# Performance work log

Measured on AMD Instinct MI355X. Metric: run time of the kernel, lower is better.

The kernel has to match this reference:

```python
import jax, jax.numpy as jnp
import numpy as np

B, P, V, E, F = 4, 8, 2048, 2048, 4096
BIG = 1e10  # stand-in for +inf that keeps gradients clean


def setup_inputs() -> dict:
    key = jax.random.key(0)
    ks = jax.random.split(key, 8)
    xs = jax.random.normal(ks[0], (B, V, 3), jnp.float32)
    # Projection matrices: random rows for x/y, third (depth) row kept near
    # [0,0,0,2] so the perspective divide is well conditioned for randn verts.
    pm = 0.5 * jax.random.normal(ks[1], (P, 3, 4), jnp.float32)
    pm = pm.at[:, 2, :3].set(0.01 * jax.random.normal(ks[2], (P, 3), jnp.float32))
    pm = pm.at[:, 2, 3].set(2.0)
    edgemaps = jax.random.normal(ks[3], (B, P, E, 2), jnp.float32)
    edgemap_lengths = jax.random.randint(ks[4], (B, P), E // 2, E + 1)
    boundary_mask = jax.random.randint(ks[5], (B, P, V), 0, 2).astype(bool)
    faces = jax.random.randint(ks[6], (B, F, 3), 0, V)
    target_volumes = 10.0 * jax.random.normal(ks[7], (B,), jnp.float32)
    return dict(xs=xs, projmatrices=pm, edgemaps=edgemaps,
                edgemap_lengths=edgemap_lengths, boundary_mask=boundary_mask,
                faces=faces, target_volumes=target_volumes)


def _silhouette_chamfer(xs, projmatrices, edgemaps, edgemap_lengths, boundary_mask):
    b, v, _ = xs.shape
    xh = jnp.concatenate([xs, jnp.ones((b, v, 1), xs.dtype)], axis=-1)  # [B,V,4]
    proj = jnp.einsum('pij,bvj->bpvi', projmatrices, xh)               # [B,P,V,3]
    pts = proj[..., :2] / proj[..., 2:3]                               # [B,P,V,2]
    e = edgemaps.shape[2]
    d2 = (jnp.sum(pts * pts, -1)[..., :, None]
          + jnp.sum(edgemaps * edgemaps, -1)[..., None, :]
          - 2.0 * jnp.einsum('bpvc,bpec->bpve', pts, edgemaps))
    yvalid = jnp.arange(e)[None, None, :] < edgemap_lengths[..., None]  # [B,P,E]
    d2 = jnp.where(yvalid[:, :, None, :], d2, jnp.asarray(BIG, d2.dtype))
    mins = jnp.min(d2, axis=-1)                                        # [B,P,V]
    xm = boundary_mask.astype(d2.dtype)
    # point_reduction='mean' over valid boundary points per projection,
    # batch_reduction='mean' over the P projections of each mesh.
    per_proj = jnp.sum(mins * xm, -1) / jnp.maximum(jnp.sum(xm, -1), 1.0)  # [B,P]
    return jnp.mean(per_proj, axis=-1)                                 # [B]


def _volume_constraint(xs, faces, target_volumes):
    b = xs.shape[0]
    fv = xs[jnp.arange(b)[:, None, None], faces]   # [B,F,3,3] gather face verts
    v0, v1, v2 = fv[:, :, 0], fv[:, :, 1], fv[:, :, 2]
    face_vols = jnp.sum(jnp.cross(v0, v1) * v2, axis=-1) / 6.0  # [B,F]
    vols = jnp.abs(jnp.sum(face_vols, axis=-1))                 # scatter-add per mesh
    return (vols - target_volumes) ** 2                          # [B]


def reference(xs, projmatrices, edgemaps, edgemap_lengths, boundary_mask, faces, target_volumes):
    chamfer = _silhouette_chamfer(xs, projmatrices, edgemaps, edgemap_lengths, boundary_mask)
    vol_error = _volume_constraint(xs, faces, target_volumes)
    return chamfer, vol_error
```

## Files before the change

### kernel.cpp

```cpp
#include <hip/hip_runtime.h>

#define NB 4
#define NP 8
#define NV 2048
#define NE 2048
#define NF 4096
#define BIGV 1.0e10f
#define NCHUNK 16
#define ECHUNK 128
#define NCOMBO (NB * NP)

#define MINPART_FLOATS (NCOMBO * NCHUNK * NV)

__global__ __launch_bounds__(256) void fused_k1(
    const float* __restrict__ xs, const float* __restrict__ pm,
    const float* __restrict__ edgemaps, const int* __restrict__ elen,
    const int* __restrict__ faces, float* __restrict__ minpart,
    float* __restrict__ volpart)
{
    __shared__ float4 eds[ECHUNK];
    __shared__ float red[4];
    const int tid = threadIdx.x;
    const int bid = blockIdx.x;

    if (bid < 512) {
        const int combo  = bid >> 4;
        const int echunk = bid & 15;
        const int b = combo >> 3;
        const int p = combo & 7;

        if (tid < ECHUNK) {
            const int e   = echunk * ECHUNK + tid;
            const int len = elen[combo];
            float ex = edgemaps[((size_t)combo * NE + e) * 2 + 0];
            float ey = edgemaps[((size_t)combo * NE + e) * 2 + 1];
            float e2;
            if (e < len) {
                e2 = ex * ex + ey * ey;
            } else {
                ex = 0.0f; ey = 0.0f; e2 = BIGV;
            }
            eds[tid] = make_float4(ex, ey, e2, 0.0f);
        }

        const float* M = pm + p * 12;
        const float m00 = M[0], m01 = M[1], m02 = M[2],  m03 = M[3];
        const float m10 = M[4], m11 = M[5], m12 = M[6],  m13 = M[7];
        const float m20 = M[8], m21 = M[9], m22 = M[10], m23 = M[11];

        float px2[8], py2[8], v2[8], mn[8];
        #pragma unroll
        for (int i = 0; i < 8; i++) {
            const int v = tid + (i << 8);
            const float x = xs[((size_t)b * NV + v) * 3 + 0];
            const float y = xs[((size_t)b * NV + v) * 3 + 1];
            const float z = xs[((size_t)b * NV + v) * 3 + 2];
            const float r0 = m00 * x + m01 * y + m02 * z + m03;
            const float r1 = m10 * x + m11 * y + m12 * z + m13;
            const float r2 = m20 * x + m21 * y + m22 * z + m23;
            const float inv = 1.0f / r2;
            const float px = r0 * inv;
            const float py = r1 * inv;
            px2[i] = -2.0f * px;
            py2[i] = -2.0f * py;
            v2[i]  = px * px + py * py;
            mn[i]  = 3.0e38f;
        }
        __syncthreads();

        #pragma unroll 4
        for (int k = 0; k < ECHUNK; k++) {
            const float4 ed = eds[k];
            #pragma unroll
            for (int i = 0; i < 8; i++)
                mn[i] = fminf(mn[i], fmaf(py2[i], ed.y, fmaf(px2[i], ed.x, ed.z)));
        }

        float* dst = minpart + ((size_t)(combo * NCHUNK + echunk)) * NV;
        #pragma unroll
        for (int i = 0; i < 8; i++)
            dst[tid + (i << 8)] = mn[i] + v2[i];
    } else {
        const int j = bid - 512;
        const int b = j >> 4;
        const int f = ((j & 15) << 8) + tid;
        const int* fc = faces + ((size_t)b * NF + f) * 3;
        const int i0 = fc[0], i1 = fc[1], i2 = fc[2];
        const float* xb = xs + (size_t)b * NV * 3;
        const float ax = xb[i0 * 3 + 0], ay = xb[i0 * 3 + 1], az = xb[i0 * 3 + 2];
        const float bx = xb[i1 * 3 + 0], by = xb[i1 * 3 + 1], bz = xb[i1 * 3 + 2];
        const float cx = xb[i2 * 3 + 0], cy = xb[i2 * 3 + 1], cz = xb[i2 * 3 + 2];
        const float crx = ay * bz - az * by;
        const float cry = az * bx - ax * bz;
        const float crz = ax * by - ay * bx;
        float fv = (crx * cx + cry * cy + crz * cz) * (1.0f / 6.0f);

        #pragma unroll
        for (int off = 32; off > 0; off >>= 1) fv += __shfl_down(fv, off);
        const int lane = tid & 63, w = tid >> 6;
        if (lane == 0) red[w] = fv;
        __syncthreads();
        if (tid == 0) volpart[j] = red[0] + red[1] + red[2] + red[3];
    }
}

__global__ __launch_bounds__(256) void fused_k2(
    const float* __restrict__ minpart, const void* __restrict__ maskp,
    float* __restrict__ percombo)
{
    __shared__ float reds[4], redc[4];
    const int tid = threadIdx.x;
    const int lane = tid & 63, w = tid >> 6;
    const int combo = blockIdx.x;

    const int* mi = (const int*)maskp;
    const unsigned char* mb = (const unsigned char*)maskp;
    bool as_int = true;
    #pragma unroll
    for (int k = 0; k < 16; k++)
        if (((const unsigned*)maskp)[k] > 1u) as_int = false;

    const float* base = minpart + (size_t)combo * NCHUNK * NV;
    float s = 0.0f, c = 0.0f;
    #pragma unroll
    for (int i = 0; i < 8; i++) {
        const int v = tid + (i << 8);
        float m = base[v];
        #pragma unroll
        for (int ch = 1; ch < NCHUNK; ch++)
            m = fminf(m, base[ch * NV + v]);
        const size_t mix = (size_t)combo * NV + v;
        const float msk = as_int ? (mi[mix] ? 1.0f : 0.0f)
                                 : (mb[mix] ? 1.0f : 0.0f);
        s += m * msk;
        c += msk;
    }
    #pragma unroll
    for (int off = 32; off > 0; off >>= 1) {
        s += __shfl_down(s, off);
        c += __shfl_down(c, off);
    }
    if (lane == 0) { reds[w] = s; redc[w] = c; }
    __syncthreads();
    if (tid == 0) {
        const float S = reds[0] + reds[1] + reds[2] + reds[3];
        const float C = redc[0] + redc[1] + redc[2] + redc[3];
        percombo[combo] = S / fmaxf(C, 1.0f);
    }
}

__global__ __launch_bounds__(64) void fused_k3(
    const float* __restrict__ percombo, const float* __restrict__ volpart,
    const float* __restrict__ tv, float* __restrict__ out)
{
    const int b = threadIdx.x;
    if (b < NB) {
        float a = 0.0f;
        #pragma unroll
        for (int p = 0; p < NP; p++) a += percombo[b * NP + p];
        out[b] = a * (1.0f / NP);
        float vs = 0.0f;
        #pragma unroll
        for (int k = 0; k < 16; k++) vs += volpart[b * 16 + k];
        const float d = fabsf(vs) - tv[b];
        out[4 + b] = d * d;
    }
}

extern "C" void kernel_launch(void* const* d_in, const int* in_sizes, int n_in,
                              void* d_out, int out_size, void* d_ws, size_t ws_size,
                              hipStream_t stream)
{
    const float* xs       = (const float*)d_in[0];
    const float* pm       = (const float*)d_in[1];
    const float* edgemaps = (const float*)d_in[2];
    const int*   elen     = (const int*)d_in[3];
    const void*  mask     = d_in[4];
    const int*   faces    = (const int*)d_in[5];
    const float* tv       = (const float*)d_in[6];
    float* out = (float*)d_out;

    float* minpart  = (float*)d_ws;
    float* volpart  = minpart + MINPART_FLOATS;
    float* percombo = volpart + 64;

    fused_k1<<<dim3(576), dim3(256), 0, stream>>>(xs, pm, edgemaps, elen, faces, minpart, volpart);
    fused_k2<<<dim3(NCOMBO), dim3(256), 0, stream>>>(minpart, mask, percombo);
    fused_k3<<<dim3(1), dim3(64), 0, stream>>>(percombo, volpart, tv, out);
}
```

Baseline: 85.93 us.

## Split work by vertex chunk and reduce chamfer minima in shared memory

Each block now owns a 128-vertex chunk and loads all 2048 edge points into shared memory. Its 16 thread groups each scan a 128-edge span, then the partial minima are combined in shared memory and masked. This drops the 4MB global minpart buffer and the separate reduction kernel, merging the final kernels into one tiny kernel (two launches instead of three). The cost is larger shared memory per block (about 41KB), which may lower occupancy, plus an extra block-wide sync.

```diff
diff --git a/kernel.cpp b/kernel.cpp
--- a/kernel.cpp
+++ b/kernel.cpp
@@ -6,41 +6,46 @@
 #define NE 2048
 #define NF 4096
 #define BIGV 1.0e10f
-#define NCHUNK 16
-#define ECHUNK 128
 #define NCOMBO (NB * NP)
+#define NSPAN 16
+#define SPANE 128
+#define SPAD (SPANE + 1)
+#define NVC 16
+#define VC 128
+#define PPAD (VC + 4)
 
-#define MINPART_FLOATS (NCOMBO * NCHUNK * NV)
 
 __global__ __launch_bounds__(256) void fused_k1(
     const float* __restrict__ xs, const float* __restrict__ pm,
     const float* __restrict__ edgemaps, const int* __restrict__ elen,
-    const int* __restrict__ faces, float* __restrict__ minpart,
+    const int* __restrict__ faces, const void* __restrict__ maskp,
+    float* __restrict__ spart, float* __restrict__ cpart,
     float* __restrict__ volpart)
 {
-    __shared__ float4 eds[ECHUNK];
-    __shared__ float red[4];
+    __shared__ float4 eds[NSPAN * SPAD];
+    __shared__ float part[NSPAN][PPAD];
+    __shared__ float reds[2], redc[2], redv[4];
     const int tid = threadIdx.x;
     const int bid = blockIdx.x;
 
     if (bid < 512) {
         const int combo  = bid >> 4;
-        const int echunk = bid & 15;
+        const int vchunk = bid & 15;
         const int b = combo >> 3;
         const int p = combo & 7;
 
-        if (tid < ECHUNK) {
-            const int e   = echunk * ECHUNK + tid;
-            const int len = elen[combo];
-            float ex = edgemaps[((size_t)combo * NE + e) * 2 + 0];
-            float ey = edgemaps[((size_t)combo * NE + e) * 2 + 1];
+        const int len = elen[combo];
+        #pragma unroll
+        for (int j = 0; j < 8; j++) {
+            const int e = tid + (j << 8);
+            float2 exy = ((const float2*)edgemaps)[(size_t)combo * NE + e];
             float e2;
             if (e < len) {
-                e2 = ex * ex + ey * ey;
+                e2 = exy.x * exy.x + exy.y * exy.y;
             } else {
-                ex = 0.0f; ey = 0.0f; e2 = BIGV;
+                exy.x = 0.0f; exy.y = 0.0f; e2 = BIGV;
             }
-            eds[tid] = make_float4(ex, ey, e2, 0.0f);
+            eds[(e >> 7) * SPAD + (e & 127)] = make_float4(exy.x, exy.y, e2, 0.0f);
         }
 
         const float* M = pm + p * 12;
@@ -48,10 +53,14 @@
         const float m10 = M[4], m11 = M[5], m12 = M[6],  m13 = M[7];
         const float m20 = M[8], m21 = M[9], m22 = M[10], m23 = M[11];
 
+        const int vgroup = tid & 15;
+        const int span   = tid >> 4;
+        const int v0     = vchunk * VC + (vgroup << 3);
+
         float px2[8], py2[8], v2[8], mn[8];
         #pragma unroll
         for (int i = 0; i < 8; i++) {
-            const int v = tid + (i << 8);
+            const int v = v0 + i;
             const float x = xs[((size_t)b * NV + v) * 3 + 0];
             const float y = xs[((size_t)b * NV + v) * 3 + 1];
             const float z = xs[((size_t)b * NV + v) * 3 + 2];
@@ -68,18 +77,50 @@
         }
         __syncthreads();
 
+        const float4* ep = eds + span * SPAD;
         #pragma unroll 4
-        for (int k = 0; k < ECHUNK; k++) {
-            const float4 ed = eds[k];
+        for (int k = 0; k < SPANE; k++) {
+            const float4 ed = ep[k];
             #pragma unroll
             for (int i = 0; i < 8; i++)
                 mn[i] = fminf(mn[i], fmaf(py2[i], ed.y, fmaf(px2[i], ed.x, ed.z)));
         }
 
-        float* dst = minpart + ((size_t)(combo * NCHUNK + echunk)) * NV;
         #pragma unroll
         for (int i = 0; i < 8; i++)
-            dst[tid + (i << 8)] = mn[i] + v2[i];
+            part[span][(vgroup << 3) + i] = mn[i] + v2[i];
+
+        const unsigned* mw = (const unsigned*)maskp;
+        bool as_int = true;
+        #pragma unroll
+        for (int k = 0; k < 16; k++)
+            if (mw[k] > 1u) as_int = false;
+
+        __syncthreads();
+
+        float s = 0.0f, c = 0.0f;
+        if (tid < VC) {
+            float m = part[0][tid];
+            #pragma unroll
+            for (int sp = 1; sp < NSPAN; sp++)
+                m = fminf(m, part[sp][tid]);
+            const size_t mix = (size_t)combo * NV + vchunk * VC + tid;
+            const float msk = as_int ? (((const int*)maskp)[mix] ? 1.0f : 0.0f)
+                                     : (((const unsigned char*)maskp)[mix] ? 1.0f : 0.0f);
+            s = m * msk;
+            c = msk;
+        }
+        #pragma unroll
+        for (int off = 32; off > 0; off >>= 1) {
+            s += __shfl_down(s, off);
+            c += __shfl_down(c, off);
+        }
+        if (tid < VC && (tid & 63) == 0) { reds[tid >> 6] = s; redc[tid >> 6] = c; }
+        __syncthreads();
+        if (tid == 0) {
+            spart[bid] = reds[0] + reds[1];
+            cpart[bid] = redc[0] + redc[1];
+        }
     } else {
         const int j = bid - 512;
         const int b = j >> 4;
@@ -98,72 +139,39 @@
         #pragma unroll
         for (int off = 32; off > 0; off >>= 1) fv += __shfl_down(fv, off);
         const int lane = tid & 63, w = tid >> 6;
-        if (lane == 0) red[w] = fv;
+        if (lane == 0) redv[w] = fv;
         __syncthreads();
-        if (tid == 0) volpart[j] = red[0] + red[1] + red[2] + red[3];
+        if (tid == 0) volpart[j] = redv[0] + redv[1] + redv[2] + redv[3];
     }
 }
 
-__global__ __launch_bounds__(256) void fused_k2(
-    const float* __restrict__ minpart, const void* __restrict__ maskp,
-    float* __restrict__ percombo)
+__global__ __launch_bounds__(64) void fused_k2(
+    const float* __restrict__ spart, const float* __restrict__ cpart,
+    const float* __restrict__ volpart, const float* __restrict__ tv,
+    float* __restrict__ out)
 {
-    __shared__ float reds[4], redc[4];
+    __shared__ float pc[NCOMBO];
     const int tid = threadIdx.x;
-    const int lane = tid & 63, w = tid >> 6;
-    const int combo = blockIdx.x;
-
-    const int* mi = (const int*)maskp;
-    const unsigned char* mb = (const unsigned char*)maskp;
-    bool as_int = true;
-    #pragma unroll
-    for (int k = 0; k < 16; k++)
-        if (((const unsigned*)maskp)[k] > 1u) as_int = false;
-
-    const float* base = minpart + (size_t)combo * NCHUNK * NV;
-    float s = 0.0f, c = 0.0f;
-    #pragma unroll
-    for (int i = 0; i < 8; i++) {
-        const int v = tid + (i << 8);
-        float m = base[v];
+    if (tid < NCOMBO) {
+        float S = 0.0f, C = 0.0f;
         #pragma unroll
-        for (int ch = 1; ch < NCHUNK; ch++)
-            m = fminf(m, base[ch * NV + v]);
-        const size_t mix = (size_t)combo * NV + v;
-        const float msk = as_int ? (mi[mix] ? 1.0f : 0.0f)
-                                 : (mb[mix] ? 1.0f : 0.0f);
-        s += m * msk;
-        c += msk;
+        for (int k = 0; k < NVC; k++) {
+            S += spart[tid * NVC + k];
+            C += cpart[tid * NVC + k];
+        }
+        pc[tid] = S / fmaxf(C, 1.0f);
     }
-    #pragma unroll
-    for (int off = 32; off > 0; off >>= 1) {
-        s += __shfl_down(s, off);
-        c += __shfl_down(c, off);
-    }
-    if (lane == 0) { reds[w] = s; redc[w] = c; }
     __syncthreads();
-    if (tid == 0) {
-        const float S = reds[0] + reds[1] + reds[2] + reds[3];
-        const float C = redc[0] + redc[1] + redc[2] + redc[3];
-        percombo[combo] = S / fmaxf(C, 1.0f);
-    }
-}
-
-__global__ __launch_bounds__(64) void fused_k3(
-    const float* __restrict__ percombo, const float* __restrict__ volpart,
-    const float* __restrict__ tv, float* __restrict__ out)
-{
-    const int b = threadIdx.x;
-    if (b < NB) {
+    if (tid < NB) {
         float a = 0.0f;
         #pragma unroll
-        for (int p = 0; p < NP; p++) a += percombo[b * NP + p];
-        out[b] = a * (1.0f / NP);
+        for (int p = 0; p < NP; p++) a += pc[tid * NP + p];
+        out[tid] = a * (1.0f / NP);
         float vs = 0.0f;
         #pragma unroll
-        for (int k = 0; k < 16; k++) vs += volpart[b * 16 + k];
-        const float d = fabsf(vs) - tv[b];
-        out[4 + b] = d * d;
+        for (int k = 0; k < 16; k++) vs += volpart[tid * 16 + k];
+        const float d = fabsf(vs) - tv[tid];
+        out[4 + tid] = d * d;
     }
 }
 
@@ -180,11 +188,11 @@
     const float* tv       = (const float*)d_in[6];
     float* out = (float*)d_out;
 
-    float* minpart  = (float*)d_ws;
-    float* volpart  = minpart + MINPART_FLOATS;
-    float* percombo = volpart + 64;
+    float* spart   = (float*)d_ws;
+    float* cpart   = spart + NCOMBO * NVC;
+    float* volpart = cpart + NCOMBO * NVC;
 
-    fused_k1<<<dim3(576), dim3(256), 0, stream>>>(xs, pm, edgemaps, elen, faces, minpart, volpart);
-    fused_k2<<<dim3(NCOMBO), dim3(256), 0, stream>>>(minpart, mask, percombo);
-    fused_k3<<<dim3(1), dim3(64), 0, stream>>>(percombo, volpart, tv, out);
+    fused_k1<<<dim3(576), dim3(256), 0, stream>>>(xs, pm, edgemaps, elen, faces, mask,
+                                                  spart, cpart, volpart);
+    fused_k2<<<dim3(1), dim3(64), 0, stream>>>(spart, cpart, volpart, tv, out);
 }
```

After: 81.41 us. 1.06x faster.
